# Performance work log

Measured on AMD Instinct MI355X. Metric: run time of the kernel, lower is better.

Reference implementation:

```python
import jax, jax.numpy as jnp
import numpy as np

B, S, E, H = 2, 2048, 1024, 16
HD = E // H

def setup_inputs() -> dict:
    key = jax.random.key(0)
    ks = jax.random.split(key, 12)
    q = jax.random.normal(ks[0], (B, S, E), jnp.float32)
    k = jax.random.normal(ks[1], (B, S, E), jnp.float32)
    v = jax.random.normal(ks[2], (B, S, E), jnp.float32)
    # causal mask: 1.0 where attention is disallowed (upper triangle)
    mask = jnp.triu(jnp.ones((S, S), jnp.float32), k=1)[None, None, :, :]
    w = lambda kk: jax.random.normal(kk, (E, E), jnp.float32) * 0.02
    return {
        "q": q, "k": k, "v": v, "mask": mask,
        "Wq": w(ks[3]), "bq": jnp.zeros((E,), jnp.float32),
        "Wk": w(ks[4]), "bk": jnp.zeros((E,), jnp.float32),
        "Wv": w(ks[5]), "bv": jnp.zeros((E,), jnp.float32),
        "Wz": w(ks[6]), "bz": jnp.zeros((E,), jnp.float32),
    }

def _create_heads(x):
    # Faithful to tf.reshape(tf.transpose(x), (B, H, -1, HD)):
    # tf.transpose reverses all dims: [B,S,E] -> [E,S,B], then reshape.
    return jnp.transpose(x, (2, 1, 0)).reshape(B, H, -1, HD)

def reference(q, k, v, mask, Wq, bq, Wk, bk, Wv, bv, Wz, bz):
    qh = _create_heads(q @ Wq + bq)  # (B,H,S,HD)
    kh = _create_heads(k @ Wk + bk)
    vh = _create_heads(v @ Wv + bv)
    qn = qh / jnp.linalg.norm(qh, axis=-1, keepdims=True)
    kn = kh / jnp.linalg.norm(kh, axis=-1, keepdims=True)
    logits = jnp.einsum('bhqd,bhkd->bhqk', qn, kn) * 1000.0
    logits = logits + mask * -1000000000.0
    attn = jax.nn.softmax(logits, axis=-1)  # (B,H,S,S)
    z = jnp.einsum('bhqk,bhkd->bhqd', attn, vh)
    zc = jnp.transpose(z, (0, 2, 1, 3)).reshape(B, -1, E)
    return zc @ Wz + bz, attn
```

## Files before the change

kernel.cpp:

```cpp
#include <hip/hip_runtime.h>
#include <cstdint>
#include <cstddef>


typedef __bf16 bf16x4 __attribute__((ext_vector_type(4)));
typedef __bf16 bf16x8 __attribute__((ext_vector_type(8)));
typedef float floatx4 __attribute__((ext_vector_type(4)));

#define GLOAD_LDS16(g, l)                                                      \
    __builtin_amdgcn_global_load_lds(                                          \
        (const __attribute__((address_space(1))) void*)(g),                    \
        (__attribute__((address_space(3))) void*)(l), 16, 0, 0)

__device__ __forceinline__ void nt_store4(float* p, floatx4 v) {
    __builtin_nontemporal_store(v, (floatx4*)p);
}

#define LOG2E_1000 1442.6950408889634f

__global__ __launch_bounds__(256) void prep(
    const float* __restrict__ x0, const float* __restrict__ x1,
    const float* __restrict__ x2, __bf16* __restrict__ ApBase,
    const float* __restrict__ w0, const float* __restrict__ w1,
    const float* __restrict__ w2, const float* __restrict__ w3,
    __bf16* __restrict__ Bp0, __bf16* __restrict__ BpzDst, int nW)
{
    const int flat = (int)blockIdx.x;
    const int tid = (int)threadIdx.x;

    if (flat < 12288) {
        const int z = flat >> 12;
        const int bx = flat & 4095;
        const float* X = z == 0 ? x0 : (z == 1 ? x1 : x2);
        __bf16* Ap = ApBase + (size_t)z * (4096ull * 2048);
        const int idx = bx * 256 + tid;
        const int r = idx >> 8;
        const int c = (idx & 255) * 4;
        float4 t = *(const float4*)(X + (size_t)r * 1024 + c);
        bf16x4 hi, lo;
        hi[0] = (__bf16)t.x; lo[0] = (__bf16)(t.x - (float)hi[0]);
        hi[1] = (__bf16)t.y; lo[1] = (__bf16)(t.y - (float)hi[1]);
        hi[2] = (__bf16)t.z; lo[2] = (__bf16)(t.z - (float)hi[2]);
        hi[3] = (__bf16)t.w; lo[3] = (__bf16)(t.w - (float)hi[3]);
        *(bf16x4*)(Ap + (size_t)r * 2048 + c) = hi;
        *(bf16x4*)(Ap + (size_t)r * 2048 + 1024 + c) = lo;
        return;
    }

    const int t = flat - 12288;
    const int slice = t >> 8;
    if (slice >= nW) return;
    const int idx = t & 255;
    const float* W = slice == 0 ? w0 : (slice == 1 ? w1 : (slice == 2 ? w2 : w3));
    __bf16* Bp = slice < 3 ? (Bp0 + (size_t)slice * (1024ull * 2048)) : BpzDst;

    __shared__ float tile[64][65];
    const int k0 = (idx >> 4) * 64, n0 = (idx & 15) * 64;
    #pragma unroll
    for (int p = 0; p < 4; ++p) {
        int kr = p * 16 + (tid >> 4);
        float4 v = *(const float4*)(W + (size_t)(k0 + kr) * 1024 + n0 + (tid & 15) * 4);
        tile[kr][(tid & 15) * 4 + 0] = v.x; tile[kr][(tid & 15) * 4 + 1] = v.y;
        tile[kr][(tid & 15) * 4 + 2] = v.z; tile[kr][(tid & 15) * 4 + 3] = v.w;
    }
    __syncthreads();
    const int nr = tid >> 2, kc = (tid & 3) * 16;
    bf16x8 hi0, hi1, lo0, lo1;
    #pragma unroll
    for (int j = 0; j < 8; ++j) {
        float x = tile[kc + j][nr];
        __bf16 h = (__bf16)x; hi0[j] = h; lo0[j] = (__bf16)(x - (float)h);
        float y = tile[kc + 8 + j][nr];
        __bf16 g = (__bf16)y; hi1[j] = g; lo1[j] = (__bf16)(y - (float)g);
    }
    __bf16* row = Bp + (size_t)(n0 + nr) * 2048;
    *(bf16x8*)(row + k0 + kc)            = hi0;
    *(bf16x8*)(row + k0 + kc + 8)        = hi1;
    *(bf16x8*)(row + 1024 + k0 + kc)     = lo0;
    *(bf16x8*)(row + 1024 + k0 + kc + 8) = lo1;
}

__global__ __launch_bounds__(256) void split_bt1(
    const float* __restrict__ W, __bf16* __restrict__ Bp)
{
    __shared__ float tile[64][65];
    const int tid = (int)threadIdx.x;
    const int k0 = blockIdx.y * 64, n0 = blockIdx.x * 64;
    #pragma unroll
    for (int p = 0; p < 4; ++p) {
        int kr = p * 16 + (tid >> 4);
        float4 v = *(const float4*)(W + (size_t)(k0 + kr) * 1024 + n0 + (tid & 15) * 4);
        tile[kr][(tid & 15) * 4 + 0] = v.x; tile[kr][(tid & 15) * 4 + 1] = v.y;
        tile[kr][(tid & 15) * 4 + 2] = v.z; tile[kr][(tid & 15) * 4 + 3] = v.w;
    }
    __syncthreads();
    const int nr = tid >> 2, kc = (tid & 3) * 16;
    bf16x8 hi0, hi1, lo0, lo1;
    #pragma unroll
    for (int j = 0; j < 8; ++j) {
        float x = tile[kc + j][nr];
        __bf16 h = (__bf16)x; hi0[j] = h; lo0[j] = (__bf16)(x - (float)h);
        float y = tile[kc + 8 + j][nr];
        __bf16 g = (__bf16)y; hi1[j] = g; lo1[j] = (__bf16)(y - (float)g);
    }
    __bf16* row = Bp + (size_t)(n0 + nr) * 2048;
    *(bf16x8*)(row + k0 + kc)            = hi0;
    *(bf16x8*)(row + k0 + kc + 8)        = hi1;
    *(bf16x8*)(row + 1024 + k0 + kc)     = lo0;
    *(bf16x8*)(row + 1024 + k0 + kc + 8) = lo1;
}

__global__ __launch_bounds__(256) void gemm_split(
    const __bf16* __restrict__ Ap0, size_t aSlice, int aStride,
    const __bf16* __restrict__ Bp0, size_t bSlice,
    const float* __restrict__ b0, const float* __restrict__ b1,
    const float* __restrict__ b2, float* __restrict__ Out0,
    int transposeOut, int chunksQK, int chunksV,
    __bf16* __restrict__ Qp, __bf16* __restrict__ Kp, int fuseQK)
{
    const int z = blockIdx.z;
    const int nch = (z == 2) ? chunksV : chunksQK;
    const bool fuse = fuseQK && (z < 2);
    const __bf16* Ap = Ap0 + (size_t)z * aSlice;
    const __bf16* Bp = Bp0 + (size_t)z * bSlice;
    const float* bias = z == 0 ? b0 : (z == 1 ? b1 : b2);
    float* Out = Out0 + (size_t)z * (4096ull * 1024);

    __shared__ __bf16 As[2 * 128 * 32];
    __shared__ __bf16 Bs[2 * 128 * 32];

    const int tid = (int)threadIdx.x;
    const int wave = tid >> 6, lane = tid & 63;
    const int quad = lane >> 4, tl = lane & 15;
    const int m0 = blockIdx.x * 128, n0 = blockIdx.y * 128;
    const int waveM = wave >> 1, waveN = wave & 1;

    floatx4 acc[4][4];
    #pragma unroll
    for (int i = 0; i < 4; ++i)
        #pragma unroll
        for (int j = 0; j < 4; ++j)
            acc[i][j] = (floatx4){0.f, 0.f, 0.f, 0.f};

    const int sRow  = (wave << 4) + (lane >> 2);
    const int sColB = (lane & 3) << 4;
    auto* AsL = (__attribute__((address_space(3))) char*)As;
    auto* BsL = (__attribute__((address_space(3))) char*)Bs;
    const int ldsOff = wave * 1024;

    size_t aRow[2];
    #pragma unroll
    for (int i = 0; i < 2; ++i) {
        const int mrow = i * 64 + sRow;
        if (fuse) {
            const int u = mrow & 63;
            aRow[i] = (size_t)((u >> 5) * 2048 + (m0 >> 1) + (mrow >> 6) * 32 + (u & 31));
        } else {
            aRow[i] = (size_t)(m0 + mrow);
        }
    }

    for (int k0 = 0; k0 < 1024; k0 += 32) {
        __syncthreads();
        #pragma unroll
        for (int i = 0; i < 2; ++i) {
            GLOAD_LDS16((const char*)(Ap + aRow[i] * aStride + k0) + sColB,
                        AsL + i * 4096 + ldsOff);
            GLOAD_LDS16((const char*)(Bp + (size_t)(n0 + i*64 + sRow) * 2048 + k0) + sColB,
                        BsL + i * 4096 + ldsOff);
            if (nch > 1) {
                GLOAD_LDS16((const char*)(Ap + 1024 + aRow[i] * aStride + k0) + sColB,
                            AsL + 8192 + i * 4096 + ldsOff);
                GLOAD_LDS16((const char*)(Bp + 1024 + (size_t)(n0 + i*64 + sRow) * 2048 + k0) + sColB,
                            BsL + 8192 + i * 4096 + ldsOff);
            }
        }
        __syncthreads();

        bf16x8 ah[4], bh[4], al[4], bl[4];
        #pragma unroll
        for (int mt = 0; mt < 4; ++mt)
            ah[mt] = *(const bf16x8*)(As + (waveM*64 + mt*16 + tl) * 32 + quad * 8);
        #pragma unroll
        for (int nt = 0; nt < 4; ++nt)
            bh[nt] = *(const bf16x8*)(Bs + (waveN*64 + nt*16 + tl) * 32 + quad * 8);
        #pragma unroll
        for (int mt = 0; mt < 4; ++mt)
            #pragma unroll
            for (int nt = 0; nt < 4; ++nt)
                acc[mt][nt] = __builtin_amdgcn_mfma_f32_16x16x32_bf16(
                    ah[mt], bh[nt], acc[mt][nt], 0, 0, 0);
        if (nch > 1) {
            #pragma unroll
            for (int mt = 0; mt < 4; ++mt)
                al[mt] = *(const bf16x8*)(As + 4096 + (waveM*64 + mt*16 + tl) * 32 + quad * 8);
            #pragma unroll
            for (int mt = 0; mt < 4; ++mt)
                #pragma unroll
                for (int nt = 0; nt < 4; ++nt)
                    acc[mt][nt] = __builtin_amdgcn_mfma_f32_16x16x32_bf16(
                        al[mt], bh[nt], acc[mt][nt], 0, 0, 0);
        }
        if (nch > 2) {
            #pragma unroll
            for (int nt = 0; nt < 4; ++nt)
                bl[nt] = *(const bf16x8*)(Bs + 4096 + (waveN*64 + nt*16 + tl) * 32 + quad * 8);
            #pragma unroll
            for (int mt = 0; mt < 4; ++mt)
                #pragma unroll
                for (int nt = 0; nt < 4; ++nt)
                    acc[mt][nt] = __builtin_amdgcn_mfma_f32_16x16x32_bf16(
                        ah[mt], bl[nt], acc[mt][nt], 0, 0, 0);
        }
    }

    if (fuse) {
        __bf16* Outp = (z == 0) ? Qp : Kp;
        const int g = ((m0 >> 7) << 1) + waveM;
        #pragma unroll
        for (int nt = 0; nt < 4; ++nt) {
            const int e = n0 + waveN * 64 + nt * 16 + tl;
            const float bb = bias[e];
            float vals[16];
            float ss = 0.f;
            #pragma unroll
            for (int mt = 0; mt < 4; ++mt)
                #pragma unroll
                for (int reg = 0; reg < 4; ++reg) {
                    float vv = acc[mt][nt][reg] + bb;
                    vals[mt * 4 + reg] = vv;
                    ss += vv * vv;
                }
            ss += __shfl_xor(ss, 16);
            ss += __shfl_xor(ss, 32);
            const float inv = 1.0f / sqrtf(ss);
            const int head = ((e >> 9) << 4) + ((e >> 5) & 15);
            const int sp = ((e & 31) << 6) + g;
            __bf16* row = Outp + ((size_t)head * 2048 + sp) * 128;
            #pragma unroll
            for (int mt = 0; mt < 2; ++mt)
                #pragma unroll
                for (int r0 = 0; r0 < 4; r0 += 2) {
                    const int d0 = (mt * 16 + quad * 4 + r0) * 2;
                    float v0 = vals[mt * 4 + r0] * inv;
                    float v1 = vals[(mt + 2) * 4 + r0] * inv;
                    float v2 = vals[mt * 4 + r0 + 1] * inv;
                    float v3 = vals[(mt + 2) * 4 + r0 + 1] * inv;
                    bf16x4 hv, lo4;
                    hv[0] = (__bf16)v0; lo4[0] = (__bf16)(v0 - (float)hv[0]);
                    hv[1] = (__bf16)v1; lo4[1] = (__bf16)(v1 - (float)hv[1]);
                    hv[2] = (__bf16)v2; lo4[2] = (__bf16)(v2 - (float)hv[2]);
                    hv[3] = (__bf16)v3; lo4[3] = (__bf16)(v3 - (float)hv[3]);
                    *(bf16x4*)(row + d0) = hv;
                    *(bf16x4*)(row + 64 + d0) = lo4;
                }
        }
    } else if (transposeOut) {
        #pragma unroll
        for (int nt = 0; nt < 4; ++nt) {
            const int e = n0 + waveN * 64 + nt * 16 + tl;
            const float bb = bias[e];
            #pragma unroll
            for (int mt = 0; mt < 4; ++mt) {
                floatx4 v = acc[mt][nt] + bb;
                *(floatx4*)(Out + (size_t)e * 4096 + m0 + waveM * 64 + mt * 16 + quad * 4) = v;
            }
        }
    } else {
        #pragma unroll
        for (int mt = 0; mt < 4; ++mt) {
            const int rbase = m0 + waveM * 64 + mt * 16 + quad * 4;
            #pragma unroll
            for (int nt = 0; nt < 4; ++nt) {
                const int e = n0 + waveN * 64 + nt * 16 + tl;
                const float bb = bias[e];
                #pragma unroll
                for (int reg = 0; reg < 4; ++reg)
                    Out[(size_t)(rbase + reg) * 1024 + e] = acc[mt][nt][reg] + bb;
            }
        }
    }
}

__global__ __launch_bounds__(256) void v_transpose(
    const float* __restrict__ PT0, __bf16* __restrict__ Vt)
{
    const int t = (int)blockIdx.x;
    const int tid = (int)threadIdx.x;
    const int st = t & 31, head = t >> 5;
    const float* PTv = PT0 + 8388608;
    const int c = (head >> 4) * 512 + (head & 15) * 32 + st;
    const float* __restrict__ row = PTv + (size_t)c * 4096;

    __shared__ float tile[64][65];
    #pragma unroll
    for (int i = 0; i < 4; ++i) {
        int o = i * 1024 + tid * 4;
        float4 v4 = *(const float4*)(row + o);
        float vals[4] = {v4.x, v4.y, v4.z, v4.w};
        #pragma unroll
        for (int e = 0; e < 4; ++e) {
            int oo = o + e;
            int d  = ((oo & 2047) & 31) * 2 + (oo >> 11);
            int sl = (oo & 2047) >> 5;
            tile[sl][d] = vals[e];
        }
    }
    __syncthreads();

    const int d = tid >> 2, jb = (tid & 3) * 16;
    bf16x8 h0, h1;
    #pragma unroll
    for (int j = 0; j < 8; ++j) {
        h0[j] = (__bf16)tile[jb + j][d];
        h1[j] = (__bf16)tile[jb + 8 + j][d];
    }
    size_t bh = ((size_t)head * 64 + d) * 2048 + st * 64 + jb;
    *(bf16x8*)(Vt + bh)     = h0;
    *(bf16x8*)(Vt + bh + 8) = h1;
}

__global__ __launch_bounds__(512, 4) void attn_mfma(
    const __bf16* __restrict__ Qp, const __bf16* __restrict__ Kp,
    const __bf16* __restrict__ Vt, float* __restrict__ Attn,
    __bf16* __restrict__ Az)
{
    const int flat = (int)blockIdx.x;
    const int head = flat & 31;
    const int idx  = flat >> 5;
    const int it   = (idx < 8) ? (15 - idx) : (idx - 8);
    const int tid = (int)threadIdx.x;
    const int w = tid >> 6, lane = tid & 63;
    const int quad = lane >> 4, tl = lane & 15;
    const int t7 = tl & 7;
    const int i0 = it * 128;
    const int jtmax = 2 * it + 1;
    const int wrowMax = i0 + w * 16 + 15;
    const int wdiag   = (i0 + w * 16) >> 6;
    const int irowBase = w * 16 + quad * 4;

    const __bf16* __restrict__ Qh = Qp + ((size_t)head * 2048 + i0) * 128;
    const __bf16* __restrict__ Kh = Kp + (size_t)head * 2048 * 128;
    const __bf16* __restrict__ Vh = Vt + (size_t)head * 64 * 2048;
    float* __restrict__ Ah = Attn + (size_t)head * ((size_t)2048 * 2048);

    __shared__ __bf16 kb[2][64 * 128];
    __shared__ __bf16 vt[2][64 * 64];
    __shared__ __bf16 ps[8][16 * 72];
    __bf16* psw = ps[w];
    auto* kbL = (__attribute__((address_space(3))) char*)&kb[0][0];
    auto* vtL = (__attribute__((address_space(3))) char*)&vt[0][0];

    const char* kSrc[2];
    #pragma unroll
    for (int i = 0; i < 2; ++i) {
        int d  = i * 512 + tid;
        int rK = d >> 4, cK = (d & 15) ^ (rK & 7);
        kSrc[i] = (const char*)(Kh + (size_t)rK * 128) + cK * 16;
    }
    const char* vSrc;
    {
        int rV = tid >> 3, cV = (tid & 7) ^ (rV & 7);
        vSrc = (const char*)(Vh + (size_t)rV * 2048) + cV * 16;
    }
    const int ok0 = ((quad)      ^ t7) * 8;
    const int ok1 = ((quad + 4)  ^ t7) * 8;
    const int ok2 = ((quad + 8)  ^ t7) * 8;
    const int ok3 = ((quad + 12) ^ t7) * 8;

    const __bf16* qrow = Qh + (size_t)(w * 16 + tl) * 128;
    bf16x8 qhi0 = *(const bf16x8*)(qrow + quad * 8);
    bf16x8 qhi1 = *(const bf16x8*)(qrow + 32 + quad * 8);
    bf16x8 qlo0 = *(const bf16x8*)(qrow + 64 + quad * 8);
    bf16x8 qlo1 = *(const bf16x8*)(qrow + 96 + quad * 8);

    for (int jt = jtmax + 1; jt < 32; ++jt) {
        floatx4 z4 = (floatx4){0.f, 0.f, 0.f, 0.f};
        #pragma unroll
        for (int g = 0; g < 4; ++g)
            nt_store4(Ah + (size_t)(i0 + w * 16 + g * 4 + quad) * 2048
                          + jt * 64 + tl * 4, z4);
    }

    float m[4], l[4];
    #pragma unroll
    for (int r = 0; r < 4; ++r) { m[r] = -3.0e38f; l[r] = 0.0f; }

    #pragma unroll
    for (int i = 0; i < 2; ++i)
        GLOAD_LDS16(kSrc[i], kbL + i * 8192 + w * 1024);

    for (int jt = 0; jt <= jtmax; ++jt) {
        const int cur = jt & 1;
        __syncthreads();
        if (jt < jtmax) {
            #pragma unroll
            for (int i = 0; i < 2; ++i)
                GLOAD_LDS16(kSrc[i] + (size_t)(jt + 1) * 16384,
                            kbL + (cur ^ 1) * 16384 + i * 8192 + w * 1024);
        }
        if (jt * 64 > wrowMax) continue;

        const __bf16* kbuf = &kb[cur][0];
        const bool diag = (jt == wdiag);
        #pragma unroll
        for (int sub = 0; sub < 4; ++sub) {
            const __bf16* kr = kbuf + (sub * 16 + tl) * 128;
            bf16x8 khi0 = *(const bf16x8*)(kr + ok0);
            bf16x8 khi1 = *(const bf16x8*)(kr + ok1);
            bf16x8 klo0 = *(const bf16x8*)(kr + ok2);
            bf16x8 klo1 = *(const bf16x8*)(kr + ok3);
            floatx4 s = (floatx4){0.f, 0.f, 0.f, 0.f};
            s = __builtin_amdgcn_mfma_f32_16x16x32_bf16(qhi0, khi0, s, 0, 0, 0);
            s = __builtin_amdgcn_mfma_f32_16x16x32_bf16(qhi1, khi1, s, 0, 0, 0);
            s = __builtin_amdgcn_mfma_f32_16x16x32_bf16(qhi0, klo0, s, 0, 0, 0);
            s = __builtin_amdgcn_mfma_f32_16x16x32_bf16(qhi1, klo1, s, 0, 0, 0);
            s = __builtin_amdgcn_mfma_f32_16x16x32_bf16(qlo0, khi0, s, 0, 0, 0);
            s = __builtin_amdgcn_mfma_f32_16x16x32_bf16(qlo1, khi1, s, 0, 0, 0);
            const int col = jt * 64 + sub * 16 + tl;
            #pragma unroll
            for (int reg = 0; reg < 4; ++reg) {
                float lv = s[reg] * LOG2E_1000;
                if (diag && (col > i0 + irowBase + reg)) lv = -1.0e9f;
                float mn = fmaxf(m[reg], lv);
                l[reg] = l[reg] * exp2f(m[reg] - mn) + exp2f(lv - mn);
                m[reg] = mn;
            }
        }
    }

    #pragma unroll
    for (int reg = 0; reg < 4; ++reg) {
        #pragma unroll
        for (int mk = 8; mk >= 1; mk >>= 1) {
            float mo = __shfl_xor(m[reg], mk);
            float lo = __shfl_xor(l[reg], mk);
            float mn = fmaxf(m[reg], mo);
            l[reg] = l[reg] * exp2f(m[reg] - mn) + lo * exp2f(mo - mn);
            m[reg] = mn;
        }
    }
    float inv_l[4];
    #pragma unroll
    for (int reg = 0; reg < 4; ++reg) inv_l[reg] = 1.0f / l[reg];

    floatx4 zacc[4];
    #pragma unroll
    for (int t = 0; t < 4; ++t) zacc[t] = (floatx4){0.f, 0.f, 0.f, 0.f};

    #pragma unroll
    for (int i = 0; i < 2; ++i)
        GLOAD_LDS16(kSrc[i], kbL + i * 8192 + w * 1024);
    GLOAD_LDS16(vSrc, vtL + w * 1024);

    for (int jt = 0; jt <= jtmax; ++jt) {
        const int cur = jt & 1;
        __syncthreads();
        if (jt < jtmax) {
            #pragma unroll
            for (int i = 0; i < 2; ++i)
                GLOAD_LDS16(kSrc[i] + (size_t)(jt + 1) * 16384,
                            kbL + (cur ^ 1) * 16384 + i * 8192 + w * 1024);
            GLOAD_LDS16(vSrc + (size_t)(jt + 1) * 128,
                        vtL + (cur ^ 1) * 8192 + w * 1024);
        }

        if (jt * 64 > wrowMax) {
            floatx4 z4 = (floatx4){0.f, 0.f, 0.f, 0.f};
            #pragma unroll
            for (int g = 0; g < 4; ++g)
                nt_store4(Ah + (size_t)(i0 + w * 16 + g * 4 + quad) * 2048
                              + jt * 64 + tl * 4, z4);
            continue;
        }

        const __bf16* kbuf = &kb[cur][0];
        const __bf16* vbuf = &vt[cur][0];
        const bool diag = (jt == wdiag);
        #pragma unroll
        for (int sub = 0; sub < 4; ++sub) {
            const __bf16* kr = kbuf + (sub * 16 + tl) * 128;
            bf16x8 khi0 = *(const bf16x8*)(kr + ok0);
            bf16x8 khi1 = *(const bf16x8*)(kr + ok1);
            bf16x8 klo0 = *(const bf16x8*)(kr + ok2);
            bf16x8 klo1 = *(const bf16x8*)(kr + ok3);
            floatx4 s = (floatx4){0.f, 0.f, 0.f, 0.f};
            s = __builtin_amdgcn_mfma_f32_16x16x32_bf16(qhi0, khi0, s, 0, 0, 0);
            s = __builtin_amdgcn_mfma_f32_16x16x32_bf16(qhi1, khi1, s, 0, 0, 0);
            s = __builtin_amdgcn_mfma_f32_16x16x32_bf16(qhi0, klo0, s, 0, 0, 0);
            s = __builtin_amdgcn_mfma_f32_16x16x32_bf16(qhi1, klo1, s, 0, 0, 0);
            s = __builtin_amdgcn_mfma_f32_16x16x32_bf16(qlo0, khi0, s, 0, 0, 0);
            s = __builtin_amdgcn_mfma_f32_16x16x32_bf16(qlo1, khi1, s, 0, 0, 0);
            const int col = jt * 64 + sub * 16 + tl;
            #pragma unroll
            for (int reg = 0; reg < 4; ++reg) {
                float lv = s[reg] * LOG2E_1000;
                if (diag && (col > i0 + irowBase + reg)) lv = -1.0e9f;
                float p = exp2f(lv - m[reg]) * inv_l[reg];
                psw[(quad * 4 + reg) * 72 + sub * 16 + tl] = (__bf16)p;
            }
        }
        __asm__ volatile("s_waitcnt lgkmcnt(0)" ::: "memory");

        #pragma unroll
        for (int g = 0; g < 4; ++g) {
            bf16x4 pv = *(const bf16x4*)(psw + (g * 4 + quad) * 72 + tl * 4);
            floatx4 f = (floatx4){(float)pv[0], (float)pv[1],
                                  (float)pv[2], (float)pv[3]};
            nt_store4(Ah + (size_t)(i0 + w * 16 + g * 4 + quad) * 2048
                          + jt * 64 + tl * 4, f);
        }

        bf16x8 p0 = *(const bf16x8*)(psw + tl * 72 + quad * 8);
        bf16x8 p1 = *(const bf16x8*)(psw + tl * 72 + 32 + quad * 8);
        #pragma unroll
        for (int t = 0; t < 4; ++t) {
            const __bf16* vh0 = vbuf + (t * 16 + tl) * 64;
            bf16x8 vhi0 = *(const bf16x8*)(vh0 + ok0);
            bf16x8 vhi1 = *(const bf16x8*)(vh0 + ok1);
            zacc[t] = __builtin_amdgcn_mfma_f32_16x16x32_bf16(p0, vhi0, zacc[t], 0, 0, 0);
            zacc[t] = __builtin_amdgcn_mfma_f32_16x16x32_bf16(p1, vhi1, zacc[t], 0, 0, 0);
        }
    }

    const int b = head >> 4, h = head & 15;
    #pragma unroll
    for (int reg = 0; reg < 4; ++reg) {
        const size_t R = (size_t)b * 2048 + i0 + w * 16 + quad * 4 + reg;
        #pragma unroll
        for (int t = 0; t < 4; ++t)
            Az[R * 1024 + h * 64 + t * 16 + tl] = (__bf16)zacc[t][reg];
    }
}

extern "C" void kernel_launch(void* const* d_in, const int* in_sizes, int n_in,
                              void* d_out, int out_size, void* d_ws, size_t ws_size,
                              hipStream_t stream) {
    (void)in_sizes; (void)n_in; (void)out_size;
    const float* q  = (const float*)d_in[0];
    const float* k  = (const float*)d_in[1];
    const float* v  = (const float*)d_in[2];
    const float* Wq = (const float*)d_in[4];  const float* bq = (const float*)d_in[5];
    const float* Wk = (const float*)d_in[6];  const float* bk = (const float*)d_in[7];
    const float* Wv = (const float*)d_in[8];  const float* bv = (const float*)d_in[9];
    const float* Wz = (const float*)d_in[10]; const float* bz = (const float*)d_in[11];

    float* out0 = (float*)d_out;
    float* attn = out0 + 4194304;

    float*  PT0 = attn;
    __bf16* Ap0 = (__bf16*)(attn + 12582912);
    __bf16* Bp0 = (__bf16*)(attn + 12582912 + 12582912);

    __bf16 *Qp, *Kp, *Vtp, *Az, *Bpz;
    const bool bigWs = ws_size >= (size_t)54525952;
    if (bigWs) {
        __bf16* ws = (__bf16*)d_ws;
        Qp = ws; Kp = ws + 8388608; Vtp = ws + 16777216; Az = ws + 20971520;
        Bpz = ws + 25165824;
    } else {
        Qp = (__bf16*)d_in[0]; Kp = (__bf16*)d_in[1]; Vtp = (__bf16*)d_in[2];
        Az = (__bf16*)d_ws;
        Bpz = (__bf16*)d_in[4];
    }

    if (bigWs) {
        prep<<<dim3(12288 + 4 * 256), 256, 0, stream>>>(
            q, k, v, Ap0, Wq, Wk, Wv, Wz, Bp0, Bpz, 4);
    } else {
        prep<<<dim3(12288 + 3 * 256), 256, 0, stream>>>(
            q, k, v, Ap0, Wq, Wk, Wv, Wz, Bp0, nullptr, 3);
        split_bt1<<<dim3(16, 16), 256, 0, stream>>>(Wz, Bpz);
    }

    gemm_split<<<dim3(32, 8, 3), 256, 0, stream>>>(
        Ap0, 4096ull*2048, 2048, Bp0, 1024ull*2048,
        bq, bk, bv, PT0, 1, 3, 1,
        Qp, Kp, 1);

    v_transpose<<<dim3(1024), 256, 0, stream>>>(PT0, Vtp);

    attn_mfma<<<dim3(512), 512, 0, stream>>>(Qp, Kp, Vtp, attn, Az);

    gemm_split<<<dim3(32, 8, 1), 256, 0, stream>>>(
        Az, 0, 1024, Bpz, 0,
        bz, bz, bz, out0, 0, 1, 1,
        nullptr, nullptr, 0);
}
```

Before: 823.6 us.

## Add 64-row output GEMM, swap grid order, and use __expf in softmax

Replaces the final output projection with a new 64x128-tile GEMM kernel launched on a 8x64 grid, giving more blocks to fill the GPU. The QKV GEMM grid is swapped so that the N dimension varies fastest, which changes L2 reuse of the A tiles. The attention softmax switches from exp2f with a folded log2e scale to __expf with a 1000 scale. The new GEMM is single-buffered with two barriers per k-step, which may expose load latency.

```diff
diff --git a/kernel.cpp b/kernel.cpp
--- a/kernel.cpp
+++ b/kernel.cpp
@@ -15,8 +15,6 @@
 __device__ __forceinline__ void nt_store4(float* p, floatx4 v) {
     __builtin_nontemporal_store(v, (floatx4*)p);
 }
-
-#define LOG2E_1000 1442.6950408889634f
 
 __global__ __launch_bounds__(256) void prep(
     const float* __restrict__ x0, const float* __restrict__ x1,
@@ -132,7 +130,7 @@
     const int tid = (int)threadIdx.x;
     const int wave = tid >> 6, lane = tid & 63;
     const int quad = lane >> 4, tl = lane & 15;
-    const int m0 = blockIdx.x * 128, n0 = blockIdx.y * 128;
+    const int m0 = blockIdx.y * 128, n0 = blockIdx.x * 128;
     const int waveM = wave >> 1, waveN = wave & 1;
 
     floatx4 acc[4][4];
@@ -278,6 +276,71 @@
                 for (int reg = 0; reg < 4; ++reg)
                     Out[(size_t)(rbase + reg) * 1024 + e] = acc[mt][nt][reg] + bb;
             }
+        }
+    }
+}
+
+__global__ __launch_bounds__(256) void gemm_out64(
+    const __bf16* __restrict__ Ap, const __bf16* __restrict__ Bp,
+    const float* __restrict__ bias, float* __restrict__ Out)
+{
+    __shared__ __bf16 As[64 * 32];
+    __shared__ __bf16 Bs[128 * 32];
+
+    const int tid = (int)threadIdx.x;
+    const int wave = tid >> 6, lane = tid & 63;
+    const int quad = lane >> 4, tl = lane & 15;
+    const int m0 = blockIdx.y * 64, n0 = blockIdx.x * 128;
+    const int wm = wave >> 1, wn = wave & 1;
+
+    floatx4 acc[2][4];
+    #pragma unroll
+    for (int i = 0; i < 2; ++i)
+        #pragma unroll
+        for (int j = 0; j < 4; ++j)
+            acc[i][j] = (floatx4){0.f, 0.f, 0.f, 0.f};
+
+    const int sRow  = (wave << 4) + (lane >> 2);
+    const int sColB = (lane & 3) << 4;
+    auto* AsL = (__attribute__((address_space(3))) char*)As;
+    auto* BsL = (__attribute__((address_space(3))) char*)Bs;
+    const int ldsOff = wave * 1024;
+
+    for (int k0 = 0; k0 < 1024; k0 += 32) {
+        __syncthreads();
+        GLOAD_LDS16((const char*)(Ap + (size_t)(m0 + sRow) * 1024 + k0) + sColB,
+                    AsL + ldsOff);
+        #pragma unroll
+        for (int i = 0; i < 2; ++i)
+            GLOAD_LDS16((const char*)(Bp + (size_t)(n0 + i*64 + sRow) * 2048 + k0) + sColB,
+                        BsL + i * 4096 + ldsOff);
+        __syncthreads();
+
+        bf16x8 ah[2], bh[4];
+        #pragma unroll
+        for (int mt = 0; mt < 2; ++mt)
+            ah[mt] = *(const bf16x8*)(As + (wm*32 + mt*16 + tl) * 32 + quad * 8);
+        #pragma unroll
+        for (int nt = 0; nt < 4; ++nt)
+            bh[nt] = *(const bf16x8*)(Bs + (wn*64 + nt*16 + tl) * 32 + quad * 8);
+        #pragma unroll
+        for (int mt = 0; mt < 2; ++mt)
+            #pragma unroll
+            for (int nt = 0; nt < 4; ++nt)
+                acc[mt][nt] = __builtin_amdgcn_mfma_f32_16x16x32_bf16(
+                    ah[mt], bh[nt], acc[mt][nt], 0, 0, 0);
+    }
+
+    #pragma unroll
+    for (int mt = 0; mt < 2; ++mt) {
+        const int rbase = m0 + wm * 32 + mt * 16 + quad * 4;
+        #pragma unroll
+        for (int nt = 0; nt < 4; ++nt) {
+            const int e = n0 + wn * 64 + nt * 16 + tl;
+            const float bb = bias[e];
+            #pragma unroll
+            for (int reg = 0; reg < 4; ++reg)
+                Out[(size_t)(rbase + reg) * 1024 + e] = acc[mt][nt][reg] + bb;
         }
     }
 }
@@ -420,10 +483,10 @@
             const int col = jt * 64 + sub * 16 + tl;
             #pragma unroll
             for (int reg = 0; reg < 4; ++reg) {
-                float lv = s[reg] * LOG2E_1000;
+                float lv = s[reg] * 1000.0f;
                 if (diag && (col > i0 + irowBase + reg)) lv = -1.0e9f;
                 float mn = fmaxf(m[reg], lv);
-                l[reg] = l[reg] * exp2f(m[reg] - mn) + exp2f(lv - mn);
+                l[reg] = l[reg] * __expf(m[reg] - mn) + __expf(lv - mn);
                 m[reg] = mn;
             }
         }
@@ -436,7 +499,7 @@
             float mo = __shfl_xor(m[reg], mk);
             float lo = __shfl_xor(l[reg], mk);
             float mn = fmaxf(m[reg], mo);
-            l[reg] = l[reg] * exp2f(m[reg] - mn) + lo * exp2f(mo - mn);
+            l[reg] = l[reg] * __expf(m[reg] - mn) + lo * __expf(mo - mn);
             m[reg] = mn;
         }
     }
@@ -494,9 +557,9 @@
             const int col = jt * 64 + sub * 16 + tl;
             #pragma unroll
             for (int reg = 0; reg < 4; ++reg) {
-                float lv = s[reg] * LOG2E_1000;
+                float lv = s[reg] * 1000.0f;
                 if (diag && (col > i0 + irowBase + reg)) lv = -1.0e9f;
-                float p = exp2f(lv - m[reg]) * inv_l[reg];
+                float p = __expf(lv - m[reg]) * inv_l[reg];
                 psw[(quad * 4 + reg) * 72 + sub * 16 + tl] = (__bf16)p;
             }
         }
@@ -573,7 +636,7 @@
         split_bt1<<<dim3(16, 16), 256, 0, stream>>>(Wz, Bpz);
     }
 
-    gemm_split<<<dim3(32, 8, 3), 256, 0, stream>>>(
+    gemm_split<<<dim3(8, 32, 3), 256, 0, stream>>>(
         Ap0, 4096ull*2048, 2048, Bp0, 1024ull*2048,
         bq, bk, bv, PT0, 1, 3, 1,
         Qp, Kp, 1);
@@ -582,8 +645,5 @@
 
     attn_mfma<<<dim3(512), 512, 0, stream>>>(Qp, Kp, Vtp, attn, Az);
 
-    gemm_split<<<dim3(32, 8, 1), 256, 0, stream>>>(
-        Az, 0, 1024, Bpz, 0,
-        bz, bz, bz, out0, 0, 1, 1,
-        nullptr, nullptr, 0);
-}
+    gemm_out64<<<dim3(8, 64), 256, 0, stream>>>(Az, Bpz, bz, out0);
+}
```

New measurement: 805.6 us. -2.2%, faster.
